# Performance work log

Hardware: AMD Instinct MI355X
Metric: run time of the kernel (lower is better)

The kernel has to match this reference:

```python
import jax, jax.numpy as jnp
import numpy as np

HEAD_DIM = 16

def setup_inputs() -> dict:
    key = jax.random.key(0)
    ks = jax.random.split(key, 9)
    dim = 256
    B, H, W = 8, 32, 32
    x  = jax.random.normal(ks[0], (B, H, W, dim), jnp.float32)
    # Conv2d weights in OIHW layout (torch convention), small init
    w3 = jax.random.normal(ks[1], (dim, dim, 1, 1), jnp.float32) * 0.05
    b3 = jax.random.normal(ks[2], (dim,), jnp.float32) * 0.01
    w5 = jax.random.normal(ks[3], (dim, dim, 3, 3), jnp.float32) * 0.02
    b5 = jax.random.normal(ks[4], (dim,), jnp.float32) * 0.01
    w7 = jax.random.normal(ks[5], (dim, dim, 5, 5), jnp.float32) * 0.01
    b7 = jax.random.normal(ks[6], (dim,), jnp.float32) * 0.01
    # nn.Linear weight: (out_features=dim, in_features=attention_dim=dim), no bias
    wp = jax.random.normal(ks[7], (dim, dim), jnp.float32) * 0.05
    return {"x": x, "w3": w3, "b3": b3, "w5": w5, "b5": b5, "w7": w7, "b7": b7, "wp": wp}

def _conv2d_same(x_nchw, w_oihw, b):
    y = jax.lax.conv_general_dilated(
        x_nchw, w_oihw, window_strides=(1, 1), padding='SAME',
        dimension_numbers=('NCHW', 'OIHW', 'NCHW'))
    return y + b[None, :, None, None]

def reference(x, w3, b3, w5, b5, w7, b7, wp):
    B, H, W, C = x.shape
    N = H * W
    nh = C // HEAD_DIM            # num_heads
    scale = HEAD_DIM ** (-0.5)
    xc = jnp.transpose(x, (0, 3, 1, 2))  # NCHW
    # q: 1x1 conv, v: 3x3 conv, k: 5x5 conv (names match the torch code)
    q = _conv2d_same(xc, w3, b3).reshape(B, nh, N, HEAD_DIM)
    v = _conv2d_same(xc, w5, b5).reshape(B, nh, N, HEAD_DIM)
    k = _conv2d_same(xc, w7, b7).reshape(B, nh, N, HEAD_DIM)
    attn = jax.nn.softmax(jnp.einsum('bhnd,bhmd->bhnm', q, k) * scale, axis=-1)
    out = jnp.einsum('bhnm,bhmd->bhnd', attn, v)        # [B, nh, N, hd]
    out = jnp.transpose(out, (0, 2, 1, 3)).reshape(B, H, W, nh * HEAD_DIM)
    return out @ wp.T                                   # Linear, no bias
```

## Files before the change

### kernel.cpp

```cpp
#include <hip/hip_runtime.h>
#include <hip/hip_bf16.h>

#define DIM 256
#define HW  1024

typedef __attribute__((ext_vector_type(8))) short short8;
typedef __attribute__((ext_vector_type(4))) float floatx4;
typedef __attribute__((ext_vector_type(16))) float floatx16;
typedef __attribute__((address_space(1))) const unsigned int g_u32;
typedef __attribute__((address_space(3))) unsigned int l_u32;

__device__ inline unsigned short f2bf(float f) {
  union { float f; unsigned u; } v;
  v.f = f;
  unsigned u = v.u;
  u += 0x7fffu + ((u >> 16) & 1u);
  return (unsigned short)(u >> 16);
}

__global__ void detect_kernel(const unsigned short* __restrict__ xr,
                              int* __restrict__ flag) {
  __shared__ int cnt;
  if (threadIdx.x == 0) cnt = 0;
  __syncthreads();
  int local = 0;
  for (int i = threadIdx.x; i < 8192; i += 256) {
    unsigned short u = xr[i];
    if ((u & 0x7F80u) == 0x7F80u) local++;
  }
  if (local) atomicAdd(&cnt, local);
  __syncthreads();
  if (threadIdx.x == 0) *flag = (cnt > 0) ? 1 : 0;
}

__device__ inline float ldin(const void* p, long i, int isf32) {
  if (isf32) return ((const float*)p)[i];
  union { unsigned u; float f; } v;
  v.u = ((unsigned)((const unsigned short*)p)[i]) << 16;
  return v.f;
}

__device__ inline void frag_repack(const void* __restrict__ w,
                                   unsigned short* __restrict__ wF, int KK,
                                   int local_blk, int t, int isf32) {
  const int idx = local_blk * 256 + t;
  const int j    = idx & 7;
  const int lane = (idx >> 3) & 63;
  const int co16 = (idx >> 9) & 15;
  const int c8   = (idx >> 13) & 7;
  const int tap  = idx >> 16;
  const int co = (co16 << 4) | (lane & 15);
  const int ci = (c8 << 5) + ((lane >> 4) << 3) + j;
  wF[idx] = f2bf(ldin(w, (long)(co * 256 + ci) * KK + tap, isf32));
}

__global__ void prep_kernel(const void* __restrict__ x,
                            const void* __restrict__ w3,
                            const void* __restrict__ b3,
                            const void* __restrict__ w5,
                            const void* __restrict__ b5,
                            const void* __restrict__ w7,
                            const void* __restrict__ b7,
                            const void* __restrict__ wp,
                            unsigned short* __restrict__ xbf,
                            unsigned short* __restrict__ wF3,
                            unsigned short* __restrict__ wF5,
                            unsigned short* __restrict__ wF7,
                            unsigned short* __restrict__ wpF,
                            float* __restrict__ bc,
                            const int* __restrict__ flag) {
  const int isf32 = *flag;
  const int bid = blockIdx.x;
  const int t = threadIdx.x;
  if (bid < 2048) {
    const int i = (bid * 256 + t) * 4;
    if (isf32) {
      const float4 v = *(const float4*)((const float*)x + i);
      ushort4 o;
      o.x = f2bf(v.x); o.y = f2bf(v.y); o.z = f2bf(v.z); o.w = f2bf(v.w);
      *(ushort4*)(xbf + i) = o;
    } else {
      *(ushort4*)(xbf + i) = *(const ushort4*)((const unsigned short*)x + i);
    }
  } else if (bid < 2304) {
    frag_repack(w3, wF3, 1, bid - 2048, t, isf32);
  } else if (bid < 4608) {
    frag_repack(w5, wF5, 9, bid - 2304, t, isf32);
  } else if (bid < 11008) {
    frag_repack(w7, wF7, 25, bid - 4608, t, isf32);
  } else if (bid < 11264) {
    frag_repack(wp, wpF, 1, bid - 11008, t, isf32);
  } else {
#pragma unroll
    for (int r = 0; r < 3; ++r) {
      const int i = r * 256 + t;
      const void* src = (i < 256) ? b3 : (i < 512) ? b5 : b7;
      bc[i] = ldin(src, i & 255, isf32);
    }
  }
}

__global__ __launch_bounds__(256, 2) void convqkv_kernel(
    const unsigned short* __restrict__ xbf,
    const unsigned short* __restrict__ wFq,
    const unsigned short* __restrict__ wFv,
    const unsigned short* __restrict__ wFk,
    const float* __restrict__ bc,
    unsigned short* __restrict__ qOut,
    unsigned short* __restrict__ vOut,
    unsigned short* __restrict__ kOut) {
  constexpr int WC = 36;
  constexpr int CELLS = 12 * WC;
  constexpr int LOADS = CELLS * 4;
  __shared__ unsigned short Xs[CELLS * 40];
  __shared__ unsigned short Bs[36 * 512];
  const int t    = threadIdx.x;
  const int bid  = blockIdx.x;
  const int cog0 = bid & 15;
  const int co0  = cog0 << 4;
  const int m0   = (bid >> 4) << 8;
  const int b    = m0 >> 10;
  const int n0   = m0 & 1023;
  const int r0   = n0 >> 5;
  const int wv   = t >> 6;
  const int lane = t & 63;
  const int l15  = lane & 15;
  const int quad = lane >> 4;

  floatx4 aq[4] = {}, av[4] = {}, ak[4] = {};

  for (int c8 = 0; c8 < 8; ++c8) {
    uint4 xreg[7];
#pragma unroll
    for (int rr = 0; rr < 7; ++rr) {
      const int id = rr * 256 + t;
      const int cell = id >> 2, part = id & 3;
      const int hr = cell / WC, wc = cell - hr * WC;
      const int xr = r0 + hr - 2, xc = wc - 2;
      const bool ok = (id < LOADS) && ((unsigned)xr < 32u) &&
                      ((unsigned)xc < 32u);
      const int cr = xr < 0 ? 0 : (xr > 31 ? 31 : xr);
      const int cc = xc < 0 ? 0 : (xc > 31 ? 31 : xc);
      uint4 v = *(const uint4*)&xbf[(((b * 32 + cr) * 32 + cc) << 8) +
                                    (c8 << 5) + (part << 3)];
      if (!ok) v = make_uint4(0, 0, 0, 0);
      xreg[rr] = v;
    }
    __syncthreads();
#pragma unroll
    for (int rr = 0; rr < 9; ++rr) {
      const int tap = (rr << 2) + wv;
      if (tap < 35) {
        const unsigned short* src;
        if (tap < 25) {
          src = &wFk[((((tap << 3) + c8) << 4) + cog0) * 512];
        } else if (tap < 34) {
          src = &wFv[(((((tap - 25) << 3) + c8) << 4) + cog0) * 512];
        } else {
          src = &wFq[((c8 << 4) + cog0) * 512];
        }
        __builtin_amdgcn_global_load_lds((g_u32*)(src + (lane << 3)),
                                         (l_u32*)&Bs[tap << 9], 16, 0, 0);
      }
    }
#pragma unroll
    for (int rr = 0; rr < 7; ++rr) {
      const int id = rr * 256 + t;
      if (id < LOADS)
        *(uint4*)&Xs[(id >> 2) * 40 + ((id & 3) << 3)] = xreg[rr];
    }
    __syncthreads();

#pragma unroll
    for (int tap = 0; tap < 25; ++tap) {
      const int kh = tap / 5, kw = tap % 5;
      const bool vv = (kh >= 1 && kh <= 3 && kw >= 1 && kw <= 3);
      short8 a[4];
#pragma unroll
      for (int rr2 = 0; rr2 < 2; ++rr2) {
#pragma unroll
        for (int ch = 0; ch < 2; ++ch) {
          const unsigned short* xs =
              &Xs[(((wv << 1) + rr2 + kh) * WC + (ch << 4) + l15 + kw) * 40 +
                  (quad << 3)];
          a[(rr2 << 1) + ch] = *(const short8*)xs;
        }
      }
      const short8 kb = *(const short8*)&Bs[(tap << 9) + (lane << 3)];
#pragma unroll
      for (int f = 0; f < 4; ++f)
        ak[f] = __builtin_amdgcn_mfma_f32_16x16x32_bf16(a[f], kb, ak[f],
                                                        0, 0, 0);
      if (vv) {
        const int vt = (kh - 1) * 3 + (kw - 1);
        const short8 vb = *(const short8*)&Bs[((25 + vt) << 9) + (lane << 3)];
#pragma unroll
        for (int f = 0; f < 4; ++f)
          av[f] = __builtin_amdgcn_mfma_f32_16x16x32_bf16(a[f], vb, av[f],
                                                          0, 0, 0);
      }
      if (tap == 12) {
        const short8 qb = *(const short8*)&Bs[(34 << 9) + (lane << 3)];
#pragma unroll
        for (int f = 0; f < 4; ++f)
          aq[f] = __builtin_amdgcn_mfma_f32_16x16x32_bf16(a[f], qb, aq[f],
                                                          0, 0, 0);
      }
    }
  }
#pragma unroll
  for (int rr2 = 0; rr2 < 2; ++rr2) {
#pragma unroll
    for (int ch = 0; ch < 2; ++ch) {
      const int f = (rr2 << 1) + ch;
      const int co = co0 + l15;
      const int slab = (b << 4) + (co >> 4);
      const int clo = co & 15;
      const int nb = n0 + (wv << 6) + (rr2 << 5) + (ch << 4) + (quad << 2);
      {
        const float bj = bc[co];
        floatx4 a = aq[f];
        ushort4 pk4;
        pk4.x = f2bf(a[0] + bj); pk4.y = f2bf(a[1] + bj);
        pk4.z = f2bf(a[2] + bj); pk4.w = f2bf(a[3] + bj);
        *(ushort4*)&qOut[(slab << 14) + (clo << 10) + nb] = pk4;
      }
      {
        const float bj = bc[512 + co];
        floatx4 a = ak[f];
        ushort4 pk4;
        pk4.x = f2bf(a[0] + bj); pk4.y = f2bf(a[1] + bj);
        pk4.z = f2bf(a[2] + bj); pk4.w = f2bf(a[3] + bj);
        *(ushort4*)&kOut[(slab << 14) + (clo << 10) + nb] = pk4;
      }
      {
        const float bj = bc[256 + co];
        floatx4 a = av[f];
        const int base = (slab << 14) + (clo << 6);
#pragma unroll
        for (int i = 0; i < 4; ++i) {
          const int n = nb + i;
          vOut[base + ((n & 15) << 10) + (n >> 4)] = f2bf(a[i] + bj);
        }
      }
    }
  }
}

__global__ __launch_bounds__(256) void attn_mfma_kernel(
    const unsigned short* __restrict__ qg,
    const unsigned short* __restrict__ kg,
    const unsigned short* __restrict__ vg,
    unsigned short* __restrict__ out2) {
  __shared__ __align__(16) unsigned short Kc[16384];
  __shared__ __align__(16) unsigned short Vt[16][1032];
  __shared__ __align__(16) unsigned short Pb[4][32][40];
  __shared__ float lb[4][32];
  const int t    = threadIdx.x;
  const int w    = t >> 6;
  const int lane = t & 63;
  const int slab = blockIdx.x >> 3;
  const int rb   = blockIdx.x & 7;
  const int b = slab >> 4;
  const int h = slab & 15;
  const int l31  = lane & 31;
  const int hl   = lane >> 5;
  const int l15  = lane & 15;
  const int quad = lane >> 4;

#pragma unroll
  for (int j = 0; j < 8; ++j) {
    const int id = (j << 8) + t;
    const int e  = id << 3;
    *(uint4*)&Kc[e] = *(const uint4*)&kg[(slab << 14) + e];
    const int d = e >> 10, ky = e & 1023;
    *(uint4*)&Vt[d][ky] = *(const uint4*)&vg[(slab << 14) + e];
  }

  const int row0 = (rb << 7) + (w << 5);
  const short8 qa =
      *(const short8*)&qg[(slab << 14) + ((row0 + l31) << 4) + (hl << 3)];

  float lsum[16] = {};
  floatx4 acco[2] = {};
  const float sc = 0.25f * 1.4426950408889634f;

  __syncthreads();

  for (int kc = 0; kc < 1024; kc += 32) {
    const short8 kb = *(const short8*)&Kc[((kc + l31) << 4) + (hl << 3)];
    floatx16 s = {};
    s = __builtin_amdgcn_mfma_f32_32x32x16_bf16(qa, kb, s, 0, 0, 0);
#pragma unroll
    for (int r = 0; r < 16; ++r) {
      const float e = exp2f(s[r] * sc);
      lsum[r] += e;
      const int row = (r & 3) + ((r >> 2) << 3) + (hl << 2);
      Pb[w][row][l31] = f2bf(e);
    }
    const short8 vb = *(const short8*)&Vt[l15][kc + (quad << 3)];
#pragma unroll
    for (int tt = 0; tt < 2; ++tt) {
      const short8 pa = *(const short8*)&Pb[w][(tt << 4) + l15][quad << 3];
      acco[tt] =
          __builtin_amdgcn_mfma_f32_16x16x32_bf16(pa, vb, acco[tt], 0, 0, 0);
    }
  }

#pragma unroll
  for (int r = 0; r < 16; ++r) {
    float lv = lsum[r];
    lv += __shfl_xor(lv, 1, 64);
    lv += __shfl_xor(lv, 2, 64);
    lv += __shfl_xor(lv, 4, 64);
    lv += __shfl_xor(lv, 8, 64);
    lv += __shfl_xor(lv, 16, 64);
    lsum[r] = lv;
  }
  {
    const int rr = l31;
    if (((rr >> 2) & 1) == hl) {
      const int reg = (rr & 3) + ((rr >> 3) << 2);
      lb[w][rr] = 1.0f / lsum[reg];
    }
  }
#pragma unroll
  for (int tt = 0; tt < 2; ++tt) {
#pragma unroll
    for (int r = 0; r < 4; ++r) {
      const int nloc = (tt << 4) + (quad << 2) + r;
      const float val = acco[tt][r] * lb[w][nloc];
      const int n = row0 + nloc;
      out2[(((b << 10) + n) << 8) + (h << 4) + l15] = f2bf(val);
    }
  }
}

__global__ __launch_bounds__(256) void linear_mfma_kernel(
    const unsigned short* __restrict__ inp,
    const unsigned short* __restrict__ wpF,
    void* __restrict__ out, const int* __restrict__ flag) {
  __shared__ unsigned short As[64 * 40];
  const int isf32 = *flag;
  const int t   = threadIdx.x;
  const int m0  = blockIdx.x << 6;
  const int co0 = blockIdx.y << 6;
  const int wv   = t >> 6;
  const int lane = t & 63;
  const int wm = (wv & 1) << 5;
  const int wn = (wv >> 1) << 5;
  const int l15  = lane & 15;
  const int quad = lane >> 4;
  const int cogb = (co0 >> 4) + (wn >> 4);
  const int rowS = t >> 2;
  const int partS = t & 3;

  floatx4 acc[2][2] = {};

  short8 cb0, cb1;
  {
    const unsigned short* wptr = &wpF[(cogb << 9) + (lane << 3)];
    cb0 = *(const short8*)wptr;
    cb1 = *(const short8*)(wptr + 512);
  }
  for (int c8 = 0; c8 < 8; ++c8) {
    const uint4 v = *(const uint4*)&inp[((m0 + rowS) << 8) + (c8 << 5) +
                                        (partS << 3)];
    short8 nb0 = {}, nb1 = {};
    if (c8 + 1 < 8) {
      const unsigned short* wptr =
          &wpF[((((c8 + 1) << 4) + cogb) << 9) + (lane << 3)];
      nb0 = *(const short8*)wptr;
      nb1 = *(const short8*)(wptr + 512);
    }
    __syncthreads();
    *(uint4*)&As[rowS * 40 + (partS << 3)] = v;
    __syncthreads();
    const unsigned short* xs = &As[(wm + l15) * 40 + (quad << 3)];
    const short8 afr0 = *(const short8*)xs;
    const short8 afr1 = *(const short8*)(xs + 16 * 40);
    acc[0][0] = __builtin_amdgcn_mfma_f32_16x16x32_bf16(afr0, cb0,
                                                        acc[0][0], 0, 0, 0);
    acc[0][1] = __builtin_amdgcn_mfma_f32_16x16x32_bf16(afr0, cb1,
                                                        acc[0][1], 0, 0, 0);
    acc[1][0] = __builtin_amdgcn_mfma_f32_16x16x32_bf16(afr1, cb0,
                                                        acc[1][0], 0, 0, 0);
    acc[1][1] = __builtin_amdgcn_mfma_f32_16x16x32_bf16(afr1, cb1,
                                                        acc[1][1], 0, 0, 0);
    cb0 = nb0; cb1 = nb1;
  }
#pragma unroll
  for (int mi = 0; mi < 2; ++mi) {
#pragma unroll
    for (int ni = 0; ni < 2; ++ni) {
      const int co = co0 + wn + (ni << 4) + l15;
      const int mb = m0 + wm + (mi << 4) + (quad << 2);
      floatx4 a = acc[mi][ni];
      if (!isf32) {
        unsigned short* o16 = (unsigned short*)out;
#pragma unroll
        for (int r = 0; r < 4; ++r) o16[(mb + r) * 256 + co] = f2bf(a[r]);
      } else {
        float* o32 = (float*)out;
#pragma unroll
        for (int r = 0; r < 4; ++r) o32[(mb + r) * 256 + co] = a[r];
      }
    }
  }
}

extern "C" void kernel_launch(void* const* d_in, const int* in_sizes, int n_in,
                              void* d_out, int out_size, void* d_ws,
                              size_t ws_size, hipStream_t stream) {
  const void* x  = d_in[0];
  const void* w3 = d_in[1];
  const void* b3 = d_in[2];
  const void* w5 = d_in[3];
  const void* b5 = d_in[4];
  const void* w7 = d_in[5];
  const void* b7 = d_in[6];
  const void* wp = d_in[7];

  char* p = (char*)d_ws;
  int* flag = (int*)p;                       p += 256;
  unsigned short* xbf = (unsigned short*)p;  p += 4u * 1024 * 1024;
  unsigned short* wF3 = (unsigned short*)p;  p += 131072;
  unsigned short* wF5 = (unsigned short*)p;  p += 1179648;
  unsigned short* wF7 = (unsigned short*)p;  p += 3276800;
  unsigned short* wpF = (unsigned short*)p;  p += 131072;
  float* bc = (float*)p;                     p += 4096;
  unsigned short* qc  = (unsigned short*)p;  p += 4194304;
  unsigned short* kT  = (unsigned short*)p;  p += 4194304;
  unsigned short* vT  = (unsigned short*)p;  p += 4194304;
  unsigned short* o2b = (unsigned short*)p;  p += 4194304;

  detect_kernel<<<1, 256, 0, stream>>>((const unsigned short*)x, flag);

  prep_kernel<<<11265, 256, 0, stream>>>(x, w3, b3, w5, b5, w7, b7, wp, xbf,
                                         wF3, wF5, wF7, wpF, bc, flag);

  convqkv_kernel<<<512, 256, 0, stream>>>(xbf, wF3, wF5, wF7, bc, qc, vT, kT);

  attn_mfma_kernel<<<1024, 256, 0, stream>>>(qc, kT, vT, o2b);

  dim3 lg(128, 4);
  linear_mfma_kernel<<<lg, 256, 0, stream>>>(o2b, wpF, d_out, flag);
}
```

Baseline: 195.7 us.

## Fold softmax scale into Q, compute row sums via MFMA, drop LDS K/V staging

The softmax scale and log2e factor move into the Q projection epilogue, so the exp loop no longer multiplies. Row sums are now computed by an extra MFMA of the bf16 probabilities against a vector of ones, which replaces the per-lane sums, the cross-lane shuffle reduction and the reciprocal table in LDS. K and V are read straight from global memory instead of being staged in about 65 KB of shared memory, and the launch bounds request 4 blocks per CU to raise occupancy. In exchange, each wave fetches K/V from global/L2 on every iteration, and the sums now come from bf16-rounded probabilities rather than fp32 ones.

New measurement: 181.2 us. -7.4%, faster.

```diff
diff --git a/kernel.cpp b/kernel.cpp
--- a/kernel.cpp
+++ b/kernel.cpp
@@ -9,6 +9,8 @@
 typedef __attribute__((ext_vector_type(16))) float floatx16;
 typedef __attribute__((address_space(1))) const unsigned int g_u32;
 typedef __attribute__((address_space(3))) unsigned int l_u32;
+
+#define QSCALE 0.36067376022224085f
 
 __device__ inline unsigned short f2bf(float f) {
   union { float f; unsigned u; } v;
@@ -221,8 +223,10 @@
         const float bj = bc[co];
         floatx4 a = aq[f];
         ushort4 pk4;
-        pk4.x = f2bf(a[0] + bj); pk4.y = f2bf(a[1] + bj);
-        pk4.z = f2bf(a[2] + bj); pk4.w = f2bf(a[3] + bj);
+        pk4.x = f2bf((a[0] + bj) * QSCALE);
+        pk4.y = f2bf((a[1] + bj) * QSCALE);
+        pk4.z = f2bf((a[2] + bj) * QSCALE);
+        pk4.w = f2bf((a[3] + bj) * QSCALE);
         *(ushort4*)&qOut[(slab << 14) + (clo << 10) + nb] = pk4;
       }
       {
@@ -247,15 +251,12 @@
   }
 }
 
-__global__ __launch_bounds__(256) void attn_mfma_kernel(
+__global__ __launch_bounds__(256, 4) void attn_mfma_kernel(
     const unsigned short* __restrict__ qg,
     const unsigned short* __restrict__ kg,
     const unsigned short* __restrict__ vg,
     unsigned short* __restrict__ out2) {
-  __shared__ __align__(16) unsigned short Kc[16384];
-  __shared__ __align__(16) unsigned short Vt[16][1032];
   __shared__ __align__(16) unsigned short Pb[4][32][40];
-  __shared__ float lb[4][32];
   const int t    = threadIdx.x;
   const int w    = t >> 6;
   const int lane = t & 63;
@@ -268,60 +269,36 @@
   const int l15  = lane & 15;
   const int quad = lane >> 4;
 
-#pragma unroll
-  for (int j = 0; j < 8; ++j) {
-    const int id = (j << 8) + t;
-    const int e  = id << 3;
-    *(uint4*)&Kc[e] = *(const uint4*)&kg[(slab << 14) + e];
-    const int d = e >> 10, ky = e & 1023;
-    *(uint4*)&Vt[d][ky] = *(const uint4*)&vg[(slab << 14) + e];
-  }
+  const unsigned short* Kb = kg + (slab << 14);
+  const unsigned short* Vb = vg + (slab << 14);
 
   const int row0 = (rb << 7) + (w << 5);
   const short8 qa =
       *(const short8*)&qg[(slab << 14) + ((row0 + l31) << 4) + (hl << 3)];
 
-  float lsum[16] = {};
-  floatx4 acco[2] = {};
-  const float sc = 0.25f * 1.4426950408889634f;
-
-  __syncthreads();
+  const short onebf = (short)0x3F80;
+  const short8 ones = {onebf, onebf, onebf, onebf, onebf, onebf, onebf, onebf};
+
+  floatx4 acco[2] = {}, asum[2] = {};
 
   for (int kc = 0; kc < 1024; kc += 32) {
-    const short8 kb = *(const short8*)&Kc[((kc + l31) << 4) + (hl << 3)];
+    const short8 kb = *(const short8*)&Kb[((kc + l31) << 4) + (hl << 3)];
     floatx16 s = {};
     s = __builtin_amdgcn_mfma_f32_32x32x16_bf16(qa, kb, s, 0, 0, 0);
 #pragma unroll
     for (int r = 0; r < 16; ++r) {
-      const float e = exp2f(s[r] * sc);
-      lsum[r] += e;
+      const float e = exp2f(s[r]);
       const int row = (r & 3) + ((r >> 2) << 3) + (hl << 2);
       Pb[w][row][l31] = f2bf(e);
     }
-    const short8 vb = *(const short8*)&Vt[l15][kc + (quad << 3)];
+    const short8 vb = *(const short8*)&Vb[(l15 << 10) + kc + (quad << 3)];
 #pragma unroll
     for (int tt = 0; tt < 2; ++tt) {
       const short8 pa = *(const short8*)&Pb[w][(tt << 4) + l15][quad << 3];
       acco[tt] =
           __builtin_amdgcn_mfma_f32_16x16x32_bf16(pa, vb, acco[tt], 0, 0, 0);
-    }
-  }
-
-#pragma unroll
-  for (int r = 0; r < 16; ++r) {
-    float lv = lsum[r];
-    lv += __shfl_xor(lv, 1, 64);
-    lv += __shfl_xor(lv, 2, 64);
-    lv += __shfl_xor(lv, 4, 64);
-    lv += __shfl_xor(lv, 8, 64);
-    lv += __shfl_xor(lv, 16, 64);
-    lsum[r] = lv;
-  }
-  {
-    const int rr = l31;
-    if (((rr >> 2) & 1) == hl) {
-      const int reg = (rr & 3) + ((rr >> 3) << 2);
-      lb[w][rr] = 1.0f / lsum[reg];
+      asum[tt] =
+          __builtin_amdgcn_mfma_f32_16x16x32_bf16(pa, ones, asum[tt], 0, 0, 0);
     }
   }
 #pragma unroll
@@ -329,7 +306,7 @@
 #pragma unroll
     for (int r = 0; r < 4; ++r) {
       const int nloc = (tt << 4) + (quad << 2) + r;
-      const float val = acco[tt][r] * lb[w][nloc];
+      const float val = acco[tt][r] / asum[tt][r];
       const int n = row0 + nloc;
       out2[(((b << 10) + n) << 8) + (h << 4) + l15] = f2bf(val);
     }
```
